# Performance work log

Measured on AMD Instinct MI355X. Metric: run time of the kernel, lower is better.

The kernel has to match this reference:

```python
import jax, jax.numpy as jnp
import numpy as np


def setup_inputs() -> dict:
    key = jax.random.key(0)
    k1, k2 = jax.random.split(key)
    x = jax.random.normal(k1, (32, 256, 56, 56), dtype=jnp.float32)
    conv_w = jax.random.normal(k2, (1, 2, 7, 7), dtype=jnp.float32) * 0.1
    return {"x": x, "conv_w": conv_w}


def reference(x, conv_w):
    # channel-wise mean and max, keepdim -> [B,1,H,W] each
    avg_out = jnp.mean(x, axis=1, keepdims=True)
    max_out = jnp.max(x, axis=1, keepdims=True)
    y = jnp.concatenate([avg_out, max_out], axis=1)  # [B,2,H,W]
    pad = (conv_w.shape[-1] - 1) // 2
    y = jax.lax.conv_general_dilated(
        y, conv_w,
        window_strides=(1, 1),
        padding=[(pad, pad), (pad, pad)],
        dimension_numbers=("NCHW", "OIHW", "NCHW"),
    )  # [B,1,H,W]
    y = jax.nn.sigmoid(y)
    return x * y
```

## Files before the change

kernel.cpp:

```cpp
#include <hip/hip_runtime.h>
#include <math.h>

#define BN    32
#define CN    256
#define HN    56
#define WN    56
#define HWN   (HN * WN)
#define CHWN  (CN * HWN)
#define NPOS  (BN * HWN)
#define KCH   8
#define CPK   (CN / KCH)
#define NP4   (NPOS / 4)
#define P4BLK (NP4 / 256)

typedef float fx4 __attribute__((ext_vector_type(4)));

__global__ __launch_bounds__(256) void sa_reduce_part(const float* __restrict__ x,
                                                      fx4* __restrict__ psum,
                                                      fx4* __restrict__ pmax) {
    int k  = blockIdx.x / P4BLK;
    int pb = blockIdx.x - k * P4BLK;
    int p4 = pb * 256 + threadIdx.x;
    int e  = p4 * 4;
    int b  = e / HWN;
    int s  = e - b * HWN;
    const fx4* xp = (const fx4*)(x + (size_t)b * CHWN + (size_t)(k * CPK) * HWN + s);
    fx4 sum = {0.f, 0.f, 0.f, 0.f};
    fx4 m = {-INFINITY, -INFINITY, -INFINITY, -INFINITY};
#pragma unroll
    for (int c = 0; c < CPK; ++c) {
        fx4 v = xp[c * (HWN / 4)];
        sum += v;
        m.x = fmaxf(m.x, v.x);
        m.y = fmaxf(m.y, v.y);
        m.z = fmaxf(m.z, v.z);
        m.w = fmaxf(m.w, v.w);
    }
    psum[(size_t)k * NP4 + p4] = sum;
    pmax[(size_t)k * NP4 + p4] = m;
}

__global__ __launch_bounds__(256) void sa_combine(const fx4* __restrict__ psum,
                                                  const fx4* __restrict__ pmax,
                                                  fx4* __restrict__ avg,
                                                  fx4* __restrict__ mx) {
    int p4 = blockIdx.x * 256 + threadIdx.x;
    fx4 sum = psum[p4];
    fx4 m = pmax[p4];
#pragma unroll
    for (int k = 1; k < KCH; ++k) {
        fx4 s2 = psum[(size_t)k * NP4 + p4];
        fx4 m2 = pmax[(size_t)k * NP4 + p4];
        sum += s2;
        m.x = fmaxf(m.x, m2.x);
        m.y = fmaxf(m.y, m2.y);
        m.z = fmaxf(m.z, m2.z);
        m.w = fmaxf(m.w, m2.w);
    }
    avg[p4] = sum * (1.0f / (float)CN);
    mx[p4] = m;
}

__global__ __launch_bounds__(256) void sa_conv(const float* __restrict__ avg,
                                               const float* __restrict__ mx,
                                               const float* __restrict__ cw,
                                               float* __restrict__ att) {
    int p = blockIdx.x * 256 + threadIdx.x;
    if (p >= NPOS) return;
    int b = p / HWN;
    int s = p - b * HWN;
    int h = s / WN;
    int w = s - h * WN;
    const float* a0 = avg + b * HWN;
    const float* m0 = mx + b * HWN;
    float acc = 0.0f;
#pragma unroll
    for (int kh = 0; kh < 7; ++kh) {
        int hh = h + kh - 3;
        if (hh < 0 || hh >= HN) continue;
#pragma unroll
        for (int kw = 0; kw < 7; ++kw) {
            int ww = w + kw - 3;
            if (ww < 0 || ww >= WN) continue;
            int idx = hh * WN + ww;
            acc = fmaf(cw[kh * 7 + kw],      a0[idx], acc);
            acc = fmaf(cw[49 + kh * 7 + kw], m0[idx], acc);
        }
    }
    att[p] = 1.0f / (1.0f + expf(-acc));
}

__global__ __launch_bounds__(256) void sa_mul(const fx4* __restrict__ x4,
                                              const float* __restrict__ att,
                                              fx4* __restrict__ out4) {
    int b = blockIdx.y;
    int i = blockIdx.x * 256 + threadIdx.x;
    int s = (i * 4) % HWN;
    const fx4 a = *(const fx4*)(att + b * HWN + s);
    size_t gi = (size_t)b * (CHWN / 4) + i;
    fx4 v = x4[gi];
    v *= a;
    __builtin_nontemporal_store(v, &out4[gi]);
}

extern "C" void kernel_launch(void* const* d_in, const int* in_sizes, int n_in,
                              void* d_out, int out_size, void* d_ws, size_t ws_size,
                              hipStream_t stream) {
    const float* x  = (const float*)d_in[0];
    const float* cw = (const float*)d_in[1];
    float* out = (float*)d_out;

    fx4* psum = (fx4*)d_ws;
    fx4* pmax = psum + (size_t)KCH * NP4;
    fx4* avg  = pmax + (size_t)KCH * NP4;
    fx4* mx   = avg + NP4;
    float* att = (float*)(mx + NP4);

    sa_reduce_part<<<KCH * P4BLK, 256, 0, stream>>>(x, psum, pmax);
    sa_combine<<<P4BLK, 256, 0, stream>>>(psum, pmax, avg, mx);
    sa_conv<<<NPOS / 256, 256, 0, stream>>>((const float*)avg, (const float*)mx, cw, att);

    dim3 mgrid(CHWN / 4 / 256, BN);
    sa_mul<<<mgrid, 256, 0, stream>>>((const fx4*)x, att, (fx4*)out);
}
```

Before: 208.5 us.

## Fuse combine, conv, sigmoid and multiply into one tiled kernel

Replaces the combine, 7x7 conv and multiply kernels with one kernel per (channel quarter, row tile, batch). Each block reduces the partial sums and maxes for its tile plus halo into LDS, runs the conv and sigmoid from LDS, then scales its share of x. This removes two launches and the global round trips for avg, max and attention. In exchange the halo combine and conv are recomputed across channel quarters, and the grid of 512 heavy blocks may limit memory-level parallelism.

Result: no change. 206.7 us (-0.8%).

```diff
diff --git a/kernel.cpp b/kernel.cpp
--- a/kernel.cpp
+++ b/kernel.cpp
@@ -12,6 +12,14 @@
 #define CPK   (CN / KCH)
 #define NP4   (NPOS / 4)
 #define P4BLK (NP4 / 256)
+
+#define RT_ROWS  14
+#define TILE_POS (RT_ROWS * WN)
+#define TILE_F4  (TILE_POS / 4)
+#define HALO_ROWS (RT_ROWS + 6)
+#define LDSW     62
+#define CQ       4
+#define CPQ      (CN / CQ)
 
 typedef float fx4 __attribute__((ext_vector_type(4)));
 
@@ -40,67 +48,83 @@
     pmax[(size_t)k * NP4 + p4] = m;
 }
 
-__global__ __launch_bounds__(256) void sa_combine(const fx4* __restrict__ psum,
-                                                  const fx4* __restrict__ pmax,
-                                                  fx4* __restrict__ avg,
-                                                  fx4* __restrict__ mx) {
-    int p4 = blockIdx.x * 256 + threadIdx.x;
-    fx4 sum = psum[p4];
-    fx4 m = pmax[p4];
+__global__ __launch_bounds__(256) void sa_fused(const float* __restrict__ x,
+                                                const fx4* __restrict__ psum,
+                                                const fx4* __restrict__ pmax,
+                                                const float* __restrict__ cw,
+                                                float* __restrict__ out) {
+    __shared__ float lavg[HALO_ROWS * LDSW];
+    __shared__ float lmax[HALO_ROWS * LDSW];
+    __shared__ float latt[TILE_POS];
+
+    const int t  = threadIdx.x;
+    const int cq = blockIdx.x;
+    const int rt = blockIdx.y;
+    const int b  = blockIdx.z;
+    const int r0 = rt * RT_ROWS;
+
+    for (int i = t; i < HALO_ROWS * LDSW; i += 256) {
+        lavg[i] = 0.0f;
+        lmax[i] = 0.0f;
+    }
+    __syncthreads();
+
+    for (int i = t; i < HALO_ROWS * (WN / 4); i += 256) {
+        int lr   = i / (WN / 4);
+        int col4 = i - lr * (WN / 4);
+        int gr   = r0 - 3 + lr;
+        if (gr < 0 || gr >= HN) continue;
+        int p4 = b * (HWN / 4) + gr * (WN / 4) + col4;
+        fx4 sum = psum[p4];
+        fx4 m = pmax[p4];
 #pragma unroll
-    for (int k = 1; k < KCH; ++k) {
-        fx4 s2 = psum[(size_t)k * NP4 + p4];
-        fx4 m2 = pmax[(size_t)k * NP4 + p4];
-        sum += s2;
-        m.x = fmaxf(m.x, m2.x);
-        m.y = fmaxf(m.y, m2.y);
-        m.z = fmaxf(m.z, m2.z);
-        m.w = fmaxf(m.w, m2.w);
+        for (int k = 1; k < KCH; ++k) {
+            fx4 s2 = psum[(size_t)k * NP4 + p4];
+            fx4 m2 = pmax[(size_t)k * NP4 + p4];
+            sum += s2;
+            m.x = fmaxf(m.x, m2.x);
+            m.y = fmaxf(m.y, m2.y);
+            m.z = fmaxf(m.z, m2.z);
+            m.w = fmaxf(m.w, m2.w);
+        }
+        sum *= (1.0f / (float)CN);
+        int o = lr * LDSW + 3 + col4 * 4;
+        lavg[o + 0] = sum.x; lavg[o + 1] = sum.y; lavg[o + 2] = sum.z; lavg[o + 3] = sum.w;
+        lmax[o + 0] = m.x;   lmax[o + 1] = m.y;   lmax[o + 2] = m.z;   lmax[o + 3] = m.w;
     }
-    avg[p4] = sum * (1.0f / (float)CN);
-    mx[p4] = m;
-}
+    __syncthreads();
 
-__global__ __launch_bounds__(256) void sa_conv(const float* __restrict__ avg,
-                                               const float* __restrict__ mx,
-                                               const float* __restrict__ cw,
-                                               float* __restrict__ att) {
-    int p = blockIdx.x * 256 + threadIdx.x;
-    if (p >= NPOS) return;
-    int b = p / HWN;
-    int s = p - b * HWN;
-    int h = s / WN;
-    int w = s - h * WN;
-    const float* a0 = avg + b * HWN;
-    const float* m0 = mx + b * HWN;
-    float acc = 0.0f;
+    for (int j = t; j < TILE_POS; j += 256) {
+        int h = j / WN;
+        int w = j - h * WN;
+        float acc = 0.0f;
 #pragma unroll
-    for (int kh = 0; kh < 7; ++kh) {
-        int hh = h + kh - 3;
-        if (hh < 0 || hh >= HN) continue;
+        for (int kh = 0; kh < 7; ++kh) {
 #pragma unroll
-        for (int kw = 0; kw < 7; ++kw) {
-            int ww = w + kw - 3;
-            if (ww < 0 || ww >= WN) continue;
-            int idx = hh * WN + ww;
-            acc = fmaf(cw[kh * 7 + kw],      a0[idx], acc);
-            acc = fmaf(cw[49 + kh * 7 + kw], m0[idx], acc);
+            for (int kw = 0; kw < 7; ++kw) {
+                acc = fmaf(cw[kh * 7 + kw],      lavg[(h + kh) * LDSW + w + kw], acc);
+                acc = fmaf(cw[49 + kh * 7 + kw], lmax[(h + kh) * LDSW + w + kw], acc);
+            }
         }
+        latt[j] = 1.0f / (1.0f + expf(-acc));
     }
-    att[p] = 1.0f / (1.0f + expf(-acc));
-}
+    __syncthreads();
 
-__global__ __launch_bounds__(256) void sa_mul(const fx4* __restrict__ x4,
-                                              const float* __restrict__ att,
-                                              fx4* __restrict__ out4) {
-    int b = blockIdx.y;
-    int i = blockIdx.x * 256 + threadIdx.x;
-    int s = (i * 4) % HWN;
-    const fx4 a = *(const fx4*)(att + b * HWN + s);
-    size_t gi = (size_t)b * (CHWN / 4) + i;
-    fx4 v = x4[gi];
-    v *= a;
-    __builtin_nontemporal_store(v, &out4[gi]);
+    const size_t planebase = (size_t)b * (CHWN / 4);
+    const int tilebase = r0 * (WN / 4);
+    const fx4* x4 = (const fx4*)x;
+    fx4* out4 = (fx4*)out;
+#pragma unroll 7
+    for (int it = 0; it < 49; ++it) {
+        int q = it * 256 + t;
+        int c = q / TILE_F4;
+        int s4 = q - c * TILE_F4;
+        size_t gi = planebase + (size_t)(cq * CPQ + c) * (HWN / 4) + tilebase + s4;
+        fx4 a = *(const fx4*)(latt + s4 * 4);
+        fx4 v = x4[gi];
+        v *= a;
+        __builtin_nontemporal_store(v, &out4[gi]);
+    }
 }
 
 extern "C" void kernel_launch(void* const* d_in, const int* in_sizes, int n_in,
@@ -112,14 +136,9 @@
 
     fx4* psum = (fx4*)d_ws;
     fx4* pmax = psum + (size_t)KCH * NP4;
-    fx4* avg  = pmax + (size_t)KCH * NP4;
-    fx4* mx   = avg + NP4;
-    float* att = (float*)(mx + NP4);
 
     sa_reduce_part<<<KCH * P4BLK, 256, 0, stream>>>(x, psum, pmax);
-    sa_combine<<<P4BLK, 256, 0, stream>>>(psum, pmax, avg, mx);
-    sa_conv<<<NPOS / 256, 256, 0, stream>>>((const float*)avg, (const float*)mx, cw, att);
 
-    dim3 mgrid(CHWN / 4 / 256, BN);
-    sa_mul<<<mgrid, 256, 0, stream>>>((const fx4*)x, att, (fx4*)out);
+    dim3 fgrid(CQ, HN / RT_ROWS, BN);
+    sa_fused<<<fgrid, 256, 0, stream>>>(x, psum, pmax, cw, out);
 }
```
